# Kernel tuning notes

Hardware: AMD Instinct MI355X
Metric: run time of the kernel (lower is better)

## Reference

```python
import jax, jax.numpy as jnp
import numpy as np
import jax.ops

N_NODES = 50000
N_EDGES = 800000
N_GRAPHS = 512
F_IN = 128
HID = 256
N_CLASSES = 1

def _xavier(key, shape):
    fan_in, fan_out = shape[0], shape[1]
    std = (2.0 / (fan_in + fan_out)) ** 0.5
    return jax.random.normal(key, shape, dtype=jnp.float32) * std

def setup_inputs() -> dict:
    key = jax.random.key(0)
    ks = jax.random.split(key, 12)
    x = jax.random.normal(ks[0], (N_NODES, F_IN), dtype=jnp.float32)
    edge_index = jax.random.randint(ks[1], (2, N_EDGES), 0, N_NODES, dtype=jnp.int64)
    batch = jnp.sort(jax.random.randint(ks[2], (N_NODES,), 0, N_GRAPHS, dtype=jnp.int64))
    return {
        'x': x, 'edge_index': edge_index, 'batch': batch,
        'W0': _xavier(ks[3], (F_IN, HID)), 'b0': jnp.zeros((HID,), jnp.float32),
        'W1': _xavier(ks[4], (HID, HID)), 'b1': jnp.zeros((HID,), jnp.float32),
        'W2': _xavier(ks[5], (HID, HID)), 'b2': jnp.zeros((HID,), jnp.float32),
        'Wm1': _xavier(ks[6], (HID, HID)), 'bm1': jnp.zeros((HID,), jnp.float32),
        'Wm2': _xavier(ks[7], (HID, N_CLASSES)), 'bm2': jnp.zeros((N_CLASSES,), jnp.float32),
    }

def _gcn_layer(h, W, b, src, dst, deg_inv_sqrt):
    # PyG GCNConv: linear -> symmetric-normalized aggregation (with self loops) -> bias
    hw = h @ W                                        # [N, out]
    norm = deg_inv_sqrt[src] * deg_inv_sqrt[dst]      # [E]
    msg = hw[src] * norm[:, None]                     # [E, out]
    agg = jax.ops.segment_sum(msg, dst, num_segments=N_NODES)
    agg = agg + hw * (deg_inv_sqrt ** 2)[:, None]     # self-loop term
    return agg + b

def reference(x, edge_index, batch, W0, b0, W1, b1, W2, b2, Wm1, bm1, Wm2, bm2):
    src, dst = edge_index[0], edge_index[1]
    # degree with added self loops (in-degree at dst)
    deg = jax.ops.segment_sum(jnp.ones((N_EDGES,), jnp.float32), dst, num_segments=N_NODES) + 1.0
    deg_inv_sqrt = jax.lax.rsqrt(deg)
    h = jax.nn.relu(_gcn_layer(x, W0, b0, src, dst, deg_inv_sqrt))
    h = jax.nn.relu(_gcn_layer(h, W1, b1, src, dst, deg_inv_sqrt))
    h = jax.nn.relu(_gcn_layer(h, W2, b2, src, dst, deg_inv_sqrt))
    # global mean pool over graphs
    sums = jax.ops.segment_sum(h, batch, num_segments=N_GRAPHS)
    cnts = jax.ops.segment_sum(jnp.ones((N_NODES,), jnp.float32), batch, num_segments=N_GRAPHS)
    pooled = sums / jnp.maximum(cnts, 1.0)[:, None]   # [G, HID]
    out = jax.nn.relu(pooled @ Wm1 + bm1) @ Wm2 + bm2 # [G, num_classes]
    return out
```

## Files before the change

### kernel.cpp

```cpp
#include <hip/hip_runtime.h>

constexpr int N_NODES  = 50000;
constexpr int N_EDGES  = 800000;
constexpr int N_GRAPHS = 512;
constexpr int F_IN     = 128;
constexpr int HID      = 256;
constexpr int NPAD     = 50048;

typedef short short8 __attribute__((ext_vector_type(8)));
typedef float f32x4  __attribute__((ext_vector_type(4)));

__device__ __forceinline__ unsigned short f2b(float f) {
    unsigned u = __float_as_uint(f);
    u += 0x7fffu + ((u >> 16) & 1u);
    return (unsigned short)(u >> 16);
}
__device__ __forceinline__ float b2f_lo(unsigned u) { return __uint_as_float(u << 16); }
__device__ __forceinline__ float b2f_hi(unsigned u) { return __uint_as_float(u & 0xffff0000u); }

__global__ void deg_kernel(const int* __restrict__ dst, int* __restrict__ deg) {
    int e = blockIdx.x * blockDim.x + threadIdx.x;
    if (e >= N_EDGES) return;
    atomicAdd(&deg[dst[e]], 1);
}

__global__ void dis_kernel(const int* __restrict__ deg, float* __restrict__ dis) {
    int i = blockIdx.x * blockDim.x + threadIdx.x;
    if (i >= N_NODES) return;
    dis[i] = rsqrtf((float)deg[i] + 1.0f);
}

__global__ void block_sum_kernel(const int* __restrict__ deg, int* __restrict__ bsum, int n) {
    __shared__ int sm[256];
    int t = threadIdx.x, base = blockIdx.x * 1024;
    int s = 0;
    #pragma unroll
    for (int i = 0; i < 4; ++i) { int idx = base + t + i * 256; if (idx < n) s += deg[idx]; }
    sm[t] = s; __syncthreads();
    for (int o = 128; o > 0; o >>= 1) { if (t < o) sm[t] += sm[t + o]; __syncthreads(); }
    if (t == 0) bsum[blockIdx.x] = sm[0];
}

__global__ void scan_bsum_kernel(int* __restrict__ bsum, int nb) {
    __shared__ int sm[64];
    int t = threadIdx.x;
    int v = (t < nb) ? bsum[t] : 0;
    sm[t] = v; __syncthreads();
    for (int o = 1; o < 64; o <<= 1) {
        int a = (t >= o) ? sm[t - o] : 0; __syncthreads();
        sm[t] += a; __syncthreads();
    }
    if (t < nb) bsum[t] = sm[t] - v;
}

__global__ void scan_local_kernel(const int* __restrict__ deg, const int* __restrict__ bsum,
                                  int* __restrict__ row_start, int* __restrict__ cursor, int n) {
    __shared__ int sm[256];
    int t = threadIdx.x, base = blockIdx.x * 1024;
    int idx0 = base + t * 4;
    int v[4], s = 0;
    #pragma unroll
    for (int i = 0; i < 4; ++i) { int id = idx0 + i; v[i] = (id < n) ? deg[id] : 0; s += v[i]; }
    sm[t] = s; __syncthreads();
    for (int o = 1; o < 256; o <<= 1) {
        int a = (t >= o) ? sm[t - o] : 0; __syncthreads();
        sm[t] += a; __syncthreads();
    }
    int excl = bsum[blockIdx.x] + sm[t] - s;
    #pragma unroll
    for (int i = 0; i < 4; ++i) {
        int id = idx0 + i;
        if (id < n) { row_start[id] = excl; cursor[id] = excl; }
        excl += v[i];
    }
    if (blockIdx.x == gridDim.x - 1 && t == 255) row_start[n] = excl;
}

__global__ void fill_csr(const int* __restrict__ src, const int* __restrict__ dst,
                         const float* __restrict__ dis, int* __restrict__ cursor,
                         int2* __restrict__ csr) {
    int e = blockIdx.x * blockDim.x + threadIdx.x;
    if (e >= N_EDGES) return;
    int s = src[e], d = dst[e];
    int pos = atomicAdd(&cursor[d], 1);
    float w = dis[s] * dis[d];
    csr[pos] = make_int2(s, __float_as_int(w));
}

__global__ void conv_bf16_kernel(const float* __restrict__ in, unsigned short* __restrict__ out, int n4) {
    int i = blockIdx.x * blockDim.x + threadIdx.x;
    if (i >= n4) return;
    float4 v = *reinterpret_cast<const float4*>(in + (size_t)i * 4);
    unsigned r0 = (unsigned)f2b(v.x) | ((unsigned)f2b(v.y) << 16);
    unsigned r1 = (unsigned)f2b(v.z) | ((unsigned)f2b(v.w) << 16);
    uint2 r = make_uint2(r0, r1);
    *reinterpret_cast<uint2*>(out + (size_t)i * 4) = r;
}

__global__ void wt_kernel(const float* __restrict__ W, unsigned short* __restrict__ Wt, int K) {
    int i = blockIdx.x * blockDim.x + threadIdx.x;
    if (i >= K * 256) return;
    int k = i >> 8, n = i & 255;
    Wt[n * K + k] = f2b(W[i]);
}

template<int F>
__global__ __launch_bounds__(256) void agg_bf16(
    const unsigned short* __restrict__ hin, const int* __restrict__ row_start,
    const int2* __restrict__ csr, const float* __restrict__ dis,
    unsigned short* __restrict__ out)
{
    constexpr int UV = F / 128;
    const int lane = threadIdx.x & 63;
    const int node = blockIdx.x * 4 + (threadIdx.x >> 6);
    if (node >= N_NODES) return;

    float a0 = 0.f, a1 = 0.f, a2 = 0.f, a3 = 0.f;
    {
        float dn = dis[node], sw = dn * dn;
        if constexpr (UV == 1) {
            unsigned u = *reinterpret_cast<const unsigned*>(hin + (size_t)node * F + lane * 2);
            a0 = b2f_lo(u) * sw; a1 = b2f_hi(u) * sw;
        } else {
            uint2 u = *reinterpret_cast<const uint2*>(hin + (size_t)node * F + lane * 4);
            a0 = b2f_lo(u.x) * sw; a1 = b2f_hi(u.x) * sw;
            a2 = b2f_lo(u.y) * sw; a3 = b2f_hi(u.y) * sw;
        }
    }

    int j = row_start[node];
    const int end = row_start[node + 1];
    for (; j + 3 < end; j += 4) {
        int2 c0 = csr[j], c1 = csr[j + 1], c2 = csr[j + 2], c3 = csr[j + 3];
        if constexpr (UV == 1) {
            unsigned u0 = *reinterpret_cast<const unsigned*>(hin + (size_t)c0.x * F + lane * 2);
            unsigned u1 = *reinterpret_cast<const unsigned*>(hin + (size_t)c1.x * F + lane * 2);
            unsigned u2 = *reinterpret_cast<const unsigned*>(hin + (size_t)c2.x * F + lane * 2);
            unsigned u3 = *reinterpret_cast<const unsigned*>(hin + (size_t)c3.x * F + lane * 2);
            float w0 = __int_as_float(c0.y), w1 = __int_as_float(c1.y);
            float w2 = __int_as_float(c2.y), w3 = __int_as_float(c3.y);
            a0 = fmaf(b2f_lo(u0), w0, a0); a1 = fmaf(b2f_hi(u0), w0, a1);
            a0 = fmaf(b2f_lo(u1), w1, a0); a1 = fmaf(b2f_hi(u1), w1, a1);
            a0 = fmaf(b2f_lo(u2), w2, a0); a1 = fmaf(b2f_hi(u2), w2, a1);
            a0 = fmaf(b2f_lo(u3), w3, a0); a1 = fmaf(b2f_hi(u3), w3, a1);
        } else {
            uint2 u0 = *reinterpret_cast<const uint2*>(hin + (size_t)c0.x * F + lane * 4);
            uint2 u1 = *reinterpret_cast<const uint2*>(hin + (size_t)c1.x * F + lane * 4);
            uint2 u2 = *reinterpret_cast<const uint2*>(hin + (size_t)c2.x * F + lane * 4);
            uint2 u3 = *reinterpret_cast<const uint2*>(hin + (size_t)c3.x * F + lane * 4);
            float w0 = __int_as_float(c0.y), w1 = __int_as_float(c1.y);
            float w2 = __int_as_float(c2.y), w3 = __int_as_float(c3.y);
            a0 = fmaf(b2f_lo(u0.x), w0, a0); a1 = fmaf(b2f_hi(u0.x), w0, a1);
            a2 = fmaf(b2f_lo(u0.y), w0, a2); a3 = fmaf(b2f_hi(u0.y), w0, a3);
            a0 = fmaf(b2f_lo(u1.x), w1, a0); a1 = fmaf(b2f_hi(u1.x), w1, a1);
            a2 = fmaf(b2f_lo(u1.y), w1, a2); a3 = fmaf(b2f_hi(u1.y), w1, a3);
            a0 = fmaf(b2f_lo(u2.x), w2, a0); a1 = fmaf(b2f_hi(u2.x), w2, a1);
            a2 = fmaf(b2f_lo(u2.y), w2, a2); a3 = fmaf(b2f_hi(u2.y), w2, a3);
            a0 = fmaf(b2f_lo(u3.x), w3, a0); a1 = fmaf(b2f_hi(u3.x), w3, a1);
            a2 = fmaf(b2f_lo(u3.y), w3, a2); a3 = fmaf(b2f_hi(u3.y), w3, a3);
        }
    }
    for (; j < end; ++j) {
        int2 c0 = csr[j];
        float w0 = __int_as_float(c0.y);
        if constexpr (UV == 1) {
            unsigned u0 = *reinterpret_cast<const unsigned*>(hin + (size_t)c0.x * F + lane * 2);
            a0 = fmaf(b2f_lo(u0), w0, a0); a1 = fmaf(b2f_hi(u0), w0, a1);
        } else {
            uint2 u0 = *reinterpret_cast<const uint2*>(hin + (size_t)c0.x * F + lane * 4);
            a0 = fmaf(b2f_lo(u0.x), w0, a0); a1 = fmaf(b2f_hi(u0.x), w0, a1);
            a2 = fmaf(b2f_lo(u0.y), w0, a2); a3 = fmaf(b2f_hi(u0.y), w0, a3);
        }
    }

    if constexpr (UV == 1) {
        unsigned r = (unsigned)f2b(a0) | ((unsigned)f2b(a1) << 16);
        *reinterpret_cast<unsigned*>(out + (size_t)node * F + lane * 2) = r;
    } else {
        uint2 r;
        r.x = (unsigned)f2b(a0) | ((unsigned)f2b(a1) << 16);
        r.y = (unsigned)f2b(a2) | ((unsigned)f2b(a3) << 16);
        *reinterpret_cast<uint2*>(out + (size_t)node * F + lane * 4) = r;
    }
}

__global__ __launch_bounds__(256) void gemm_mfma(
    const unsigned short* __restrict__ A,
    const unsigned short* __restrict__ Bt,
    const float* __restrict__ bias,
    unsigned short* __restrict__ C,
    int K, int relu)
{
    __shared__ __align__(16) unsigned short As[4 * 128 * 8];
    __shared__ __align__(16) unsigned short Bs[4 * 128 * 8];
    const int t    = threadIdx.x;
    const int lane = t & 63;
    const int w    = t >> 6;
    const int wm   = w & 1, wn = w >> 1;
    const int q    = lane >> 4, m = lane & 15;
    const int row0 = blockIdx.x * 128;
    const int col0 = blockIdx.y * 128;
    const int r_   = t >> 2, c_ = t & 3;

    f32x4 acc[4][4] = {};

    for (int k0 = 0; k0 < K; k0 += 32) {
        #pragma unroll
        for (int pass = 0; pass < 2; ++pass) {
            int r = r_ + pass * 64;
            uint4 av = *reinterpret_cast<const uint4*>(A  + (size_t)(row0 + r) * K + k0 + c_ * 8);
            uint4 bv = *reinterpret_cast<const uint4*>(Bt + (size_t)(col0 + r) * K + k0 + c_ * 8);
            *reinterpret_cast<uint4*>(&As[(c_ * 128 + r) * 8]) = av;
            *reinterpret_cast<uint4*>(&Bs[(c_ * 128 + r) * 8]) = bv;
        }
        __syncthreads();
        short8 af[4], bf[4];
        #pragma unroll
        for (int i = 0; i < 4; ++i)
            af[i] = *reinterpret_cast<const short8*>(&As[(q * 128 + wm * 64 + i * 16 + m) * 8]);
        #pragma unroll
        for (int j = 0; j < 4; ++j)
            bf[j] = *reinterpret_cast<const short8*>(&Bs[(q * 128 + wn * 64 + j * 16 + m) * 8]);
        #pragma unroll
        for (int i = 0; i < 4; ++i)
            #pragma unroll
            for (int j = 0; j < 4; ++j)
                acc[i][j] = __builtin_amdgcn_mfma_f32_16x16x32_bf16(af[i], bf[j], acc[i][j], 0, 0, 0);
        __syncthreads();
    }

    #pragma unroll
    for (int j = 0; j < 4; ++j) {
        int col = col0 + wn * 64 + j * 16 + m;
        float bj = bias[col];
        #pragma unroll
        for (int i = 0; i < 4; ++i) {
            int rowb = row0 + wm * 64 + i * 16 + q * 4;
            #pragma unroll
            for (int r = 0; r < 4; ++r) {
                float v = acc[i][j][r] + bj;
                if (relu) v = fmaxf(v, 0.f);
                C[(size_t)(rowb + r) * 256 + col] = f2b(v);
            }
        }
    }
}

__global__ void gstart_kernel(const int* __restrict__ batch, int* __restrict__ gstart) {
    int g = blockIdx.x * blockDim.x + threadIdx.x;
    if (g > N_GRAPHS) return;
    int lo = 0, hi = N_NODES;
    while (lo < hi) {
        int mid = (lo + hi) >> 1;
        if (batch[mid] < g) lo = mid + 1; else hi = mid;
    }
    gstart[g] = lo;
}

__global__ __launch_bounds__(256) void pool_kernel(const unsigned short* __restrict__ h,
                                                   const int* __restrict__ gstart,
                                                   float* __restrict__ pooled) {
    int g = blockIdx.x, t = threadIdx.x;
    int s = gstart[g], e = gstart[g + 1];
    float acc = 0.f;
    for (int n = s; n < e; ++n) acc += b2f_lo((unsigned)h[(size_t)n * HID + t]);
    float cnt = (float)(e - s);
    pooled[g * HID + t] = acc / fmaxf(cnt, 1.0f);
}

__global__ __launch_bounds__(256) void mlp_kernel(const float* __restrict__ pooled,
                                                  const float* __restrict__ Wm1,
                                                  const float* __restrict__ bm1,
                                                  const float* __restrict__ Wm2,
                                                  const float* __restrict__ bm2,
                                                  float* __restrict__ out) {
    __shared__ float p[HID];
    __shared__ float red[HID];
    int g = blockIdx.x, t = threadIdx.x;
    p[t] = pooled[g * HID + t];
    __syncthreads();
    float acc = bm1[t];
    for (int k = 0; k < HID; ++k) acc = fmaf(p[k], Wm1[k * HID + t], acc);
    float hval = fmaxf(acc, 0.f);
    red[t] = hval * Wm2[t];
    __syncthreads();
    for (int s = 128; s > 0; s >>= 1) {
        if (t < s) red[t] += red[t + s];
        __syncthreads();
    }
    if (t == 0) out[g] = red[0] + bm2[0];
}

extern "C" void kernel_launch(void* const* d_in, const int* in_sizes, int n_in,
                              void* d_out, int out_size, void* d_ws, size_t ws_size,
                              hipStream_t stream) {
    const float* x    = (const float*)d_in[0];
    const int*   ei   = (const int*)d_in[1];
    const int*   batch= (const int*)d_in[2];
    const float* W0   = (const float*)d_in[3];
    const float* b0   = (const float*)d_in[4];
    const float* W1   = (const float*)d_in[5];
    const float* b1   = (const float*)d_in[6];
    const float* W2   = (const float*)d_in[7];
    const float* b2   = (const float*)d_in[8];
    const float* Wm1  = (const float*)d_in[9];
    const float* bm1  = (const float*)d_in[10];
    const float* Wm2  = (const float*)d_in[11];
    const float* bm2  = (const float*)d_in[12];
    float* out = (float*)d_out;

    char* ws = (char*)d_ws;
    size_t off = 0;
    auto alloc = [&](size_t bytes) -> void* {
        void* p = ws + off;
        off += (bytes + 255) & ~(size_t)255;
        return p;
    };
    int*   deg       = (int*)  alloc((size_t)N_NODES * 4);
    float* dis       = (float*)alloc((size_t)N_NODES * 4);
    int*   row_start = (int*)  alloc((size_t)(N_NODES + 1) * 4);
    int*   cursor    = (int*)  alloc((size_t)N_NODES * 4);
    int*   bsum      = (int*)  alloc((size_t)64 * 4);
    int2*  csr       = (int2*) alloc((size_t)N_EDGES * 8);
    int*   gstart    = (int*)  alloc((size_t)(N_GRAPHS + 1) * 4);
    float* pooled    = (float*)alloc((size_t)N_GRAPHS * HID * 4);
    unsigned short* x_bf = (unsigned short*)alloc((size_t)N_NODES * F_IN * 2);
    unsigned short* Wt0  = (unsigned short*)alloc((size_t)F_IN * HID * 2);
    unsigned short* Wt1  = (unsigned short*)alloc((size_t)HID * HID * 2);
    unsigned short* Wt2  = (unsigned short*)alloc((size_t)HID * HID * 2);
    unsigned short* bufA = (unsigned short*)alloc((size_t)NPAD * HID * 2);
    unsigned short* bufB = (unsigned short*)alloc((size_t)NPAD * HID * 2);

    const int* src = ei;
    const int* dst = ei + N_EDGES;
    const int NB = (N_NODES + 1023) / 1024;

    hipMemsetAsync(deg, 0, (size_t)N_NODES * 4, stream);
    deg_kernel      <<<(N_EDGES + 255) / 256, 256, 0, stream>>>(dst, deg);
    dis_kernel      <<<(N_NODES + 255) / 256, 256, 0, stream>>>(deg, dis);
    block_sum_kernel<<<NB, 256, 0, stream>>>(deg, bsum, N_NODES);
    scan_bsum_kernel<<<1, 64, 0, stream>>>(bsum, NB);
    scan_local_kernel<<<NB, 256, 0, stream>>>(deg, bsum, row_start, cursor, N_NODES);
    fill_csr        <<<(N_EDGES + 255) / 256, 256, 0, stream>>>(src, dst, dis, cursor, csr);

    conv_bf16_kernel<<<(N_NODES * F_IN / 4 + 255) / 256, 256, 0, stream>>>(x, x_bf, N_NODES * F_IN / 4);
    wt_kernel<<<(F_IN * HID + 255) / 256, 256, 0, stream>>>(W0, Wt0, F_IN);
    wt_kernel<<<(HID * HID + 255) / 256, 256, 0, stream>>>(W1, Wt1, HID);
    wt_kernel<<<(HID * HID + 255) / 256, 256, 0, stream>>>(W2, Wt2, HID);

    dim3 ggrid(NPAD / 128, 2);

    agg_bf16<F_IN><<<(N_NODES + 3) / 4, 256, 0, stream>>>(x_bf, row_start, csr, dis, bufA);
    gemm_mfma<<<ggrid, 256, 0, stream>>>(bufA, Wt0, b0, bufB, F_IN, 1);

    agg_bf16<HID><<<(N_NODES + 3) / 4, 256, 0, stream>>>(bufB, row_start, csr, dis, bufA);
    gemm_mfma<<<ggrid, 256, 0, stream>>>(bufA, Wt1, b1, bufB, HID, 1);

    agg_bf16<HID><<<(N_NODES + 3) / 4, 256, 0, stream>>>(bufB, row_start, csr, dis, bufA);
    gemm_mfma<<<ggrid, 256, 0, stream>>>(bufA, Wt2, b2, bufB, HID, 1);

    gstart_kernel<<<3, 256, 0, stream>>>(batch, gstart);
    pool_kernel  <<<N_GRAPHS, HID, 0, stream>>>(bufB, gstart, pooled);
    mlp_kernel   <<<N_GRAPHS, HID, 0, stream>>>(pooled, Wm1, bm1, Wm2, bm2, out);
}
```

Before: 460.2 us.

## Fuse prep kernels, widen aggregation gathers, double-buffer GEMM, fuse pool+MLP

Merges the degree count, x-to-bf16 conversion and the three weight transposes into one prep kernel, and folds the rsqrt degree computation into the block-sum kernel. The aggregation kernel now loads 16-byte feature chunks per lane and splits each node's edge list across sub-groups of lanes, reducing with cross-lane shuffles. The GEMM is templated on K and double-buffers its LDS tiles, and the pool, gstart and MLP kernels become a single kernel. Together these cut launch count and aim to raise memory-level parallelism in the gather, at the cost of shuffle reductions and more LDS in the GEMM.

```diff
diff --git a/kernel.cpp b/kernel.cpp
--- a/kernel.cpp
+++ b/kernel.cpp
@@ -18,24 +18,40 @@
 __device__ __forceinline__ float b2f_lo(unsigned u) { return __uint_as_float(u << 16); }
 __device__ __forceinline__ float b2f_hi(unsigned u) { return __uint_as_float(u & 0xffff0000u); }
 
-__global__ void deg_kernel(const int* __restrict__ dst, int* __restrict__ deg) {
-    int e = blockIdx.x * blockDim.x + threadIdx.x;
-    if (e >= N_EDGES) return;
-    atomicAdd(&deg[dst[e]], 1);
-}
-
-__global__ void dis_kernel(const int* __restrict__ deg, float* __restrict__ dis) {
-    int i = blockIdx.x * blockDim.x + threadIdx.x;
-    if (i >= N_NODES) return;
-    dis[i] = rsqrtf((float)deg[i] + 1.0f);
-}
-
-__global__ void block_sum_kernel(const int* __restrict__ deg, int* __restrict__ bsum, int n) {
+__global__ __launch_bounds__(256) void prep_kernel(
+    const int* __restrict__ dst, int* __restrict__ deg,
+    const float* __restrict__ x, unsigned short* __restrict__ x_bf,
+    const float* __restrict__ W0, const float* __restrict__ W1, const float* __restrict__ W2,
+    unsigned short* __restrict__ Wt0, unsigned short* __restrict__ Wt1, unsigned short* __restrict__ Wt2)
+{
+    const int b = blockIdx.x, t = threadIdx.x;
+    if (b < 3125) {
+        int e = b * 256 + t;
+        atomicAdd(&deg[dst[e]], 1);
+    } else if (b < 9375) {
+        int i = (b - 3125) * 256 + t;
+        float4 v = *reinterpret_cast<const float4*>(x + (size_t)i * 4);
+        unsigned r0 = (unsigned)f2b(v.x) | ((unsigned)f2b(v.y) << 16);
+        unsigned r1 = (unsigned)f2b(v.z) | ((unsigned)f2b(v.w) << 16);
+        *reinterpret_cast<uint2*>(x_bf + (size_t)i * 4) = make_uint2(r0, r1);
+    } else {
+        int i = (b - 9375) * 256 + t;
+        if (i < 32768)        { int k = i >> 8, n = i & 255;               Wt0[n * 128 + k] = f2b(W0[i]); }
+        else if (i < 98304)   { int j = i - 32768; int k = j >> 8, n = j & 255; Wt1[n * 256 + k] = f2b(W1[j]); }
+        else                  { int j = i - 98304; int k = j >> 8, n = j & 255; Wt2[n * 256 + k] = f2b(W2[j]); }
+    }
+}
+
+__global__ void block_sum_dis_kernel(const int* __restrict__ deg, int* __restrict__ bsum,
+                                     float* __restrict__ dis, int n) {
     __shared__ int sm[256];
     int t = threadIdx.x, base = blockIdx.x * 1024;
     int s = 0;
     #pragma unroll
-    for (int i = 0; i < 4; ++i) { int idx = base + t + i * 256; if (idx < n) s += deg[idx]; }
+    for (int i = 0; i < 4; ++i) {
+        int idx = base + t + i * 256;
+        if (idx < n) { int d = deg[idx]; s += d; dis[idx] = rsqrtf((float)d + 1.0f); }
+    }
     sm[t] = s; __syncthreads();
     for (int o = 128; o > 0; o >>= 1) { if (t < o) sm[t] += sm[t + o]; __syncthreads(); }
     if (t == 0) bsum[blockIdx.x] = sm[0];
@@ -87,112 +103,101 @@
     csr[pos] = make_int2(s, __float_as_int(w));
 }
 
-__global__ void conv_bf16_kernel(const float* __restrict__ in, unsigned short* __restrict__ out, int n4) {
-    int i = blockIdx.x * blockDim.x + threadIdx.x;
-    if (i >= n4) return;
-    float4 v = *reinterpret_cast<const float4*>(in + (size_t)i * 4);
-    unsigned r0 = (unsigned)f2b(v.x) | ((unsigned)f2b(v.y) << 16);
-    unsigned r1 = (unsigned)f2b(v.z) | ((unsigned)f2b(v.w) << 16);
-    uint2 r = make_uint2(r0, r1);
-    *reinterpret_cast<uint2*>(out + (size_t)i * 4) = r;
-}
-
-__global__ void wt_kernel(const float* __restrict__ W, unsigned short* __restrict__ Wt, int K) {
-    int i = blockIdx.x * blockDim.x + threadIdx.x;
-    if (i >= K * 256) return;
-    int k = i >> 8, n = i & 255;
-    Wt[n * K + k] = f2b(W[i]);
-}
-
 template<int F>
 __global__ __launch_bounds__(256) void agg_bf16(
     const unsigned short* __restrict__ hin, const int* __restrict__ row_start,
     const int2* __restrict__ csr, const float* __restrict__ dis,
     unsigned short* __restrict__ out)
 {
-    constexpr int UV = F / 128;
+    constexpr int LPR  = F / 8;
+    constexpr int NSUB = 64 / LPR;
     const int lane = threadIdx.x & 63;
+    const int sub  = lane / LPR;
+    const int fc   = lane % LPR;
     const int node = blockIdx.x * 4 + (threadIdx.x >> 6);
     if (node >= N_NODES) return;
 
-    float a0 = 0.f, a1 = 0.f, a2 = 0.f, a3 = 0.f;
+    float acc[8];
     {
-        float dn = dis[node], sw = dn * dn;
-        if constexpr (UV == 1) {
-            unsigned u = *reinterpret_cast<const unsigned*>(hin + (size_t)node * F + lane * 2);
-            a0 = b2f_lo(u) * sw; a1 = b2f_hi(u) * sw;
-        } else {
-            uint2 u = *reinterpret_cast<const uint2*>(hin + (size_t)node * F + lane * 4);
-            a0 = b2f_lo(u.x) * sw; a1 = b2f_hi(u.x) * sw;
-            a2 = b2f_lo(u.y) * sw; a3 = b2f_hi(u.y) * sw;
-        }
-    }
-
-    int j = row_start[node];
+        float dn = dis[node];
+        float sw = (sub == 0) ? dn * dn : 0.0f;
+        uint2 u2[2];
+        *reinterpret_cast<uint4*>(u2) =
+            *reinterpret_cast<const uint4*>(hin + (size_t)node * F + fc * 8);
+        #pragma unroll
+        for (int h = 0; h < 2; ++h) {
+            acc[h * 4 + 0] = b2f_lo(u2[h].x) * sw;
+            acc[h * 4 + 1] = b2f_hi(u2[h].x) * sw;
+            acc[h * 4 + 2] = b2f_lo(u2[h].y) * sw;
+            acc[h * 4 + 3] = b2f_hi(u2[h].y) * sw;
+        }
+    }
+
+    int j = row_start[node] + sub;
     const int end = row_start[node + 1];
-    for (; j + 3 < end; j += 4) {
-        int2 c0 = csr[j], c1 = csr[j + 1], c2 = csr[j + 2], c3 = csr[j + 3];
-        if constexpr (UV == 1) {
-            unsigned u0 = *reinterpret_cast<const unsigned*>(hin + (size_t)c0.x * F + lane * 2);
-            unsigned u1 = *reinterpret_cast<const unsigned*>(hin + (size_t)c1.x * F + lane * 2);
-            unsigned u2 = *reinterpret_cast<const unsigned*>(hin + (size_t)c2.x * F + lane * 2);
-            unsigned u3 = *reinterpret_cast<const unsigned*>(hin + (size_t)c3.x * F + lane * 2);
-            float w0 = __int_as_float(c0.y), w1 = __int_as_float(c1.y);
-            float w2 = __int_as_float(c2.y), w3 = __int_as_float(c3.y);
-            a0 = fmaf(b2f_lo(u0), w0, a0); a1 = fmaf(b2f_hi(u0), w0, a1);
-            a0 = fmaf(b2f_lo(u1), w1, a0); a1 = fmaf(b2f_hi(u1), w1, a1);
-            a0 = fmaf(b2f_lo(u2), w2, a0); a1 = fmaf(b2f_hi(u2), w2, a1);
-            a0 = fmaf(b2f_lo(u3), w3, a0); a1 = fmaf(b2f_hi(u3), w3, a1);
-        } else {
-            uint2 u0 = *reinterpret_cast<const uint2*>(hin + (size_t)c0.x * F + lane * 4);
-            uint2 u1 = *reinterpret_cast<const uint2*>(hin + (size_t)c1.x * F + lane * 4);
-            uint2 u2 = *reinterpret_cast<const uint2*>(hin + (size_t)c2.x * F + lane * 4);
-            uint2 u3 = *reinterpret_cast<const uint2*>(hin + (size_t)c3.x * F + lane * 4);
-            float w0 = __int_as_float(c0.y), w1 = __int_as_float(c1.y);
-            float w2 = __int_as_float(c2.y), w3 = __int_as_float(c3.y);
-            a0 = fmaf(b2f_lo(u0.x), w0, a0); a1 = fmaf(b2f_hi(u0.x), w0, a1);
-            a2 = fmaf(b2f_lo(u0.y), w0, a2); a3 = fmaf(b2f_hi(u0.y), w0, a3);
-            a0 = fmaf(b2f_lo(u1.x), w1, a0); a1 = fmaf(b2f_hi(u1.x), w1, a1);
-            a2 = fmaf(b2f_lo(u1.y), w1, a2); a3 = fmaf(b2f_hi(u1.y), w1, a3);
-            a0 = fmaf(b2f_lo(u2.x), w2, a0); a1 = fmaf(b2f_hi(u2.x), w2, a1);
-            a2 = fmaf(b2f_lo(u2.y), w2, a2); a3 = fmaf(b2f_hi(u2.y), w2, a3);
-            a0 = fmaf(b2f_lo(u3.x), w3, a0); a1 = fmaf(b2f_hi(u3.x), w3, a1);
-            a2 = fmaf(b2f_lo(u3.y), w3, a2); a3 = fmaf(b2f_hi(u3.y), w3, a3);
-        }
-    }
-    for (; j < end; ++j) {
+    for (; j + 3 * NSUB < end; j += 4 * NSUB) {
+        int2 c[4];
+        #pragma unroll
+        for (int u = 0; u < 4; ++u) c[u] = csr[j + u * NSUB];
+        #pragma unroll
+        for (int u = 0; u < 4; ++u) {
+            float w = __int_as_float(c[u].y);
+            uint2 g[2];
+            *reinterpret_cast<uint4*>(g) =
+                *reinterpret_cast<const uint4*>(hin + (size_t)c[u].x * F + fc * 8);
+            #pragma unroll
+            for (int h = 0; h < 2; ++h) {
+                acc[h * 4 + 0] = fmaf(b2f_lo(g[h].x), w, acc[h * 4 + 0]);
+                acc[h * 4 + 1] = fmaf(b2f_hi(g[h].x), w, acc[h * 4 + 1]);
+                acc[h * 4 + 2] = fmaf(b2f_lo(g[h].y), w, acc[h * 4 + 2]);
+                acc[h * 4 + 3] = fmaf(b2f_hi(g[h].y), w, acc[h * 4 + 3]);
+            }
+        }
+    }
+    for (; j < end; j += NSUB) {
         int2 c0 = csr[j];
-        float w0 = __int_as_float(c0.y);
-        if constexpr (UV == 1) {
-            unsigned u0 = *reinterpret_cast<const unsigned*>(hin + (size_t)c0.x * F + lane * 2);
-            a0 = fmaf(b2f_lo(u0), w0, a0); a1 = fmaf(b2f_hi(u0), w0, a1);
-        } else {
-            uint2 u0 = *reinterpret_cast<const uint2*>(hin + (size_t)c0.x * F + lane * 4);
-            a0 = fmaf(b2f_lo(u0.x), w0, a0); a1 = fmaf(b2f_hi(u0.x), w0, a1);
-            a2 = fmaf(b2f_lo(u0.y), w0, a2); a3 = fmaf(b2f_hi(u0.y), w0, a3);
-        }
-    }
-
-    if constexpr (UV == 1) {
-        unsigned r = (unsigned)f2b(a0) | ((unsigned)f2b(a1) << 16);
-        *reinterpret_cast<unsigned*>(out + (size_t)node * F + lane * 2) = r;
-    } else {
-        uint2 r;
-        r.x = (unsigned)f2b(a0) | ((unsigned)f2b(a1) << 16);
-        r.y = (unsigned)f2b(a2) | ((unsigned)f2b(a3) << 16);
-        *reinterpret_cast<uint2*>(out + (size_t)node * F + lane * 4) = r;
-    }
-}
-
+        float w = __int_as_float(c0.y);
+        uint2 g[2];
+        *reinterpret_cast<uint4*>(g) =
+            *reinterpret_cast<const uint4*>(hin + (size_t)c0.x * F + fc * 8);
+        #pragma unroll
+        for (int h = 0; h < 2; ++h) {
+            acc[h * 4 + 0] = fmaf(b2f_lo(g[h].x), w, acc[h * 4 + 0]);
+            acc[h * 4 + 1] = fmaf(b2f_hi(g[h].x), w, acc[h * 4 + 1]);
+            acc[h * 4 + 2] = fmaf(b2f_lo(g[h].y), w, acc[h * 4 + 2]);
+            acc[h * 4 + 3] = fmaf(b2f_hi(g[h].y), w, acc[h * 4 + 3]);
+        }
+    }
+
+    #pragma unroll
+    for (int k = 0; k < 8; ++k) {
+        #pragma unroll
+        for (int off = LPR; off < 64; off <<= 1)
+            acc[k] += __shfl_xor(acc[k], off, 64);
+    }
+
+    if (sub == 0) {
+        uint2 r[2];
+        #pragma unroll
+        for (int h = 0; h < 2; ++h) {
+            r[h].x = (unsigned)f2b(acc[h * 4 + 0]) | ((unsigned)f2b(acc[h * 4 + 1]) << 16);
+            r[h].y = (unsigned)f2b(acc[h * 4 + 2]) | ((unsigned)f2b(acc[h * 4 + 3]) << 16);
+        }
+        *reinterpret_cast<uint4*>(out + (size_t)node * F + fc * 8) =
+            *reinterpret_cast<uint4*>(r);
+    }
+}
+
+template<int K>
 __global__ __launch_bounds__(256) void gemm_mfma(
     const unsigned short* __restrict__ A,
     const unsigned short* __restrict__ Bt,
     const float* __restrict__ bias,
     unsigned short* __restrict__ C,
-    int K, int relu)
+    int relu)
 {
-    __shared__ __align__(16) unsigned short As[4 * 128 * 8];
-    __shared__ __align__(16) unsigned short Bs[4 * 128 * 8];
+    __shared__ __align__(16) unsigned short As[2][4 * 128 * 8];
+    __shared__ __align__(16) unsigned short Bs[2][4 * 128 * 8];
     const int t    = threadIdx.x;
     const int lane = t & 63;
     const int w    = t >> 6;
@@ -204,41 +209,50 @@
 
     f32x4 acc[4][4] = {};
 
-    for (int k0 = 0; k0 < K; k0 += 32) {
+    auto stage = [&](int buf, int k0) {
         #pragma unroll
         for (int pass = 0; pass < 2; ++pass) {
             int r = r_ + pass * 64;
             uint4 av = *reinterpret_cast<const uint4*>(A  + (size_t)(row0 + r) * K + k0 + c_ * 8);
             uint4 bv = *reinterpret_cast<const uint4*>(Bt + (size_t)(col0 + r) * K + k0 + c_ * 8);
-            *reinterpret_cast<uint4*>(&As[(c_ * 128 + r) * 8]) = av;
-            *reinterpret_cast<uint4*>(&Bs[(c_ * 128 + r) * 8]) = bv;
-        }
-        __syncthreads();
+            *reinterpret_cast<uint4*>(&As[buf][(c_ * 128 + r) * 8]) = av;
+            *reinterpret_cast<uint4*>(&Bs[buf][(c_ * 128 + r) * 8]) = bv;
+        }
+    };
+
+    constexpr int NK = K / 32;
+    stage(0, 0);
+    __syncthreads();
+    #pragma unroll
+    for (int kb = 0; kb < NK; ++kb) {
+        if (kb + 1 < NK) stage((kb + 1) & 1, (kb + 1) * 32);
+        const unsigned short* as = As[kb & 1];
+        const unsigned short* bs = Bs[kb & 1];
         short8 af[4], bf[4];
         #pragma unroll
         for (int i = 0; i < 4; ++i)
-            af[i] = *reinterpret_cast<const short8*>(&As[(q * 128 + wm * 64 + i * 16 + m) * 8]);
-        #pragma unroll
-        for (int j = 0; j < 4; ++j)
-            bf[j] = *reinterpret_cast<const short8*>(&Bs[(q * 128 + wn * 64 + j * 16 + m) * 8]);
+            af[i] = *reinterpret_cast<const short8*>(&as[(q * 128 + wm * 64 + i * 16 + m) * 8]);
+        #pragma unroll
+        for (int jn = 0; jn < 4; ++jn)
+            bf[jn] = *reinterpret_cast<const short8*>(&bs[(q * 128 + wn * 64 + jn * 16 + m) * 8]);
         #pragma unroll
         for (int i = 0; i < 4; ++i)
             #pragma unroll
-            for (int j = 0; j < 4; ++j)
-                acc[i][j] = __builtin_amdgcn_mfma_f32_16x16x32_bf16(af[i], bf[j], acc[i][j], 0, 0, 0);
+            for (int jn = 0; jn < 4; ++jn)
+                acc[i][jn] = __builtin_amdgcn_mfma_f32_16x16x32_bf16(af[i], bf[jn], acc[i][jn], 0, 0, 0);
         __syncthreads();
     }
 
     #pragma unroll
-    for (int j = 0; j < 4; ++j) {
-        int col = col0 + wn * 64 + j * 16 + m;
+    for (int jn = 0; jn < 4; ++jn) {
+        int col = col0 + wn * 64 + jn * 16 + m;
         float bj = bias[col];
         #pragma unroll
         for (int i = 0; i < 4; ++i) {
             int rowb = row0 + wm * 64 + i * 16 + q * 4;
             #pragma unroll
             for (int r = 0; r < 4; ++r) {
-                float v = acc[i][j][r] + bj;
+                float v = acc[i][jn][r] + bj;
                 if (relu) v = fmaxf(v, 0.f);
                 C[(size_t)(rowb + r) * 256 + col] = f2b(v);
             }
@@ -246,46 +260,34 @@
     }
 }
 
-__global__ void gstart_kernel(const int* __restrict__ batch, int* __restrict__ gstart) {
-    int g = blockIdx.x * blockDim.x + threadIdx.x;
-    if (g > N_GRAPHS) return;
-    int lo = 0, hi = N_NODES;
-    while (lo < hi) {
-        int mid = (lo + hi) >> 1;
-        if (batch[mid] < g) lo = mid + 1; else hi = mid;
-    }
-    gstart[g] = lo;
-}
-
-__global__ __launch_bounds__(256) void pool_kernel(const unsigned short* __restrict__ h,
-                                                   const int* __restrict__ gstart,
-                                                   float* __restrict__ pooled) {
-    int g = blockIdx.x, t = threadIdx.x;
-    int s = gstart[g], e = gstart[g + 1];
+__global__ __launch_bounds__(256) void pool_mlp_kernel(
+    const unsigned short* __restrict__ h, const int* __restrict__ batch,
+    const float* __restrict__ Wm1, const float* __restrict__ bm1,
+    const float* __restrict__ Wm2, const float* __restrict__ bm2,
+    float* __restrict__ out)
+{
+    __shared__ float p[HID];
+    __shared__ float red[HID];
+    __shared__ int se[2];
+    const int g = blockIdx.x, t = threadIdx.x;
+    if (t < 2) {
+        int target = g + t;
+        int lo = 0, hi = N_NODES;
+        while (lo < hi) { int mid = (lo + hi) >> 1; if (batch[mid] < target) lo = mid + 1; else hi = mid; }
+        se[t] = lo;
+    }
+    __syncthreads();
+    const int s = se[0], e = se[1];
     float acc = 0.f;
     for (int n = s; n < e; ++n) acc += b2f_lo((unsigned)h[(size_t)n * HID + t]);
-    float cnt = (float)(e - s);
-    pooled[g * HID + t] = acc / fmaxf(cnt, 1.0f);
-}
-
-__global__ __launch_bounds__(256) void mlp_kernel(const float* __restrict__ pooled,
-                                                  const float* __restrict__ Wm1,
-                                                  const float* __restrict__ bm1,
-                                                  const float* __restrict__ Wm2,
-                                                  const float* __restrict__ bm2,
-                                                  float* __restrict__ out) {
-    __shared__ float p[HID];
-    __shared__ float red[HID];
-    int g = blockIdx.x, t = threadIdx.x;
-    p[t] = pooled[g * HID + t];
+    p[t] = acc / fmaxf((float)(e - s), 1.0f);
     __syncthreads();
-    float acc = bm1[t];
-    for (int k = 0; k < HID; ++k) acc = fmaf(p[k], Wm1[k * HID + t], acc);
-    float hval = fmaxf(acc, 0.f);
-    red[t] = hval * Wm2[t];
+    float a2 = bm1[t];
+    for (int k = 0; k < HID; ++k) a2 = fmaf(p[k], Wm1[k * HID + t], a2);
+    red[t] = fmaxf(a2, 0.f) * Wm2[t];
     __syncthreads();
-    for (int s = 128; s > 0; s >>= 1) {
-        if (t < s) red[t] += red[t + s];
+    for (int o = 128; o > 0; o >>= 1) {
+        if (t < o) red[t] += red[t + o];
         __syncthreads();
     }
     if (t == 0) out[g] = red[0] + bm2[0];
@@ -322,8 +324,6 @@
     int*   cursor    = (int*)  alloc((size_t)N_NODES * 4);
     int*   bsum      = (int*)  alloc((size_t)64 * 4);
     int2*  csr       = (int2*) alloc((size_t)N_EDGES * 8);
-    int*   gstart    = (int*)  alloc((size_t)(N_GRAPHS + 1) * 4);
-    float* pooled    = (float*)alloc((size_t)N_GRAPHS * HID * 4);
     unsigned short* x_bf = (unsigned short*)alloc((size_t)N_NODES * F_IN * 2);
     unsigned short* Wt0  = (unsigned short*)alloc((size_t)F_IN * HID * 2);
     unsigned short* Wt1  = (unsigned short*)alloc((size_t)HID * HID * 2);
@@ -336,30 +336,22 @@
     const int NB = (N_NODES + 1023) / 1024;
 
     hipMemsetAsync(deg, 0, (size_t)N_NODES * 4, stream);
-    deg_kernel      <<<(N_EDGES + 255) / 256, 256, 0, stream>>>(dst, deg);
-    dis_kernel      <<<(N_NODES + 255) / 256, 256, 0, stream>>>(deg, dis);
-    block_sum_kernel<<<NB, 256, 0, stream>>>(deg, bsum, N_NODES);
-    scan_bsum_kernel<<<1, 64, 0, stream>>>(bsum, NB);
-    scan_local_kernel<<<NB, 256, 0, stream>>>(deg, bsum, row_start, cursor, N_NODES);
-    fill_csr        <<<(N_EDGES + 255) / 256, 256, 0, stream>>>(src, dst, dis, cursor, csr);
-
-    conv_bf16_kernel<<<(N_NODES * F_IN / 4 + 255) / 256, 256, 0, stream>>>(x, x_bf, N_NODES * F_IN / 4);
-    wt_kernel<<<(F_IN * HID + 255) / 256, 256, 0, stream>>>(W0, Wt0, F_IN);
-    wt_kernel<<<(HID * HID + 255) / 256, 256, 0, stream>>>(W1, Wt1, HID);
-    wt_kernel<<<(HID * HID + 255) / 256, 256, 0, stream>>>(W2, Wt2, HID);
+    prep_kernel        <<<10015, 256, 0, stream>>>(dst, deg, x, x_bf, W0, W1, W2, Wt0, Wt1, Wt2);
+    block_sum_dis_kernel<<<NB, 256, 0, stream>>>(deg, bsum, dis, N_NODES);
+    scan_bsum_kernel   <<<1, 64, 0, stream>>>(bsum, NB);
+    scan_local_kernel  <<<NB, 256, 0, stream>>>(deg, bsum, row_start, cursor, N_NODES);
+    fill_csr           <<<(N_EDGES + 255) / 256, 256, 0, stream>>>(src, dst, dis, cursor, csr);
 
     dim3 ggrid(NPAD / 128, 2);
 
     agg_bf16<F_IN><<<(N_NODES + 3) / 4, 256, 0, stream>>>(x_bf, row_start, csr, dis, bufA);
-    gemm_mfma<<<ggrid, 256, 0, stream>>>(bufA, Wt0, b0, bufB, F_IN, 1);
+    gemm_mfma<F_IN><<<ggrid, 256, 0, stream>>>(bufA, Wt0, b0, bufB, 1);
 
     agg_bf16<HID><<<(N_NODES + 3) / 4, 256, 0, stream>>>(bufB, row_start, csr, dis, bufA);
-    gemm_mfma<<<ggrid, 256, 0, stream>>>(bufA, Wt1, b1, bufB, HID, 1);
+    gemm_mfma<HID><<<ggrid, 256, 0, stream>>>(bufA, Wt1, b1, bufB, 1);
 
     agg_bf16<HID><<<(N_NODES + 3) / 4, 256, 0, stream>>>(bufB, row_start, csr, dis, bufA);
-    gemm_mfma<<<ggrid, 256, 0, stream>>>(bufA, Wt2, b2, bufB, HID, 1);
-
-    gstart_kernel<<<3, 256, 0, stream>>>(batch, gstart);
-    pool_kernel  <<<N_GRAPHS, HID, 0, stream>>>(bufB, gstart, pooled);
-    mlp_kernel   <<<N_GRAPHS, HID, 0, stream>>>(pooled, Wm1, bm1, Wm2, bm2, out);
-}
+    gemm_mfma<HID><<<ggrid, 256, 0, stream>>>(bufA, Wt2, b2, bufB, 1);
+
+    pool_mlp_kernel<<<N_GRAPHS, HID, 0, stream>>>(bufB, batch, Wm1, bm1, Wm2, bm2, out);
+}
```

Result: faster. 435.8 us (-5.3%).
